# Performance work log

Hardware: AMD Instinct MI355X
Metric: run time of the kernel (lower is better)

Reference implementation:

```python
import jax, jax.numpy as jnp
import numpy as np

B, N, E, DM, DN, H = 8, 128, 2, 128, 128, 4
NEG = -1000000.0


def setup_inputs() -> dict:
    key = jax.random.key(0)
    k1, k2, k3, k4 = jax.random.split(key, 4)
    edge_msgs = jax.random.normal(k1, (B, N, N, E, DM), dtype=jnp.float32)
    node_states = jax.random.normal(k2, (B, N, DN), dtype=jnp.float32)
    edges = jax.random.randint(k3, (B, N, N, E + 1), 0, 2).astype(jnp.int32)
    # Dense(1) kernel per head over concat([edge_msgs, node_states]) -> [H, DM+DN]
    W = jax.random.normal(k4, (H, DM + DN), dtype=jnp.float32) * 0.05
    b = jnp.zeros((H,), dtype=jnp.float32)
    return {"edge_msgs": edge_msgs, "node_states": node_states, "W": W, "b": b, "edges": edges}


def reference(edge_msgs, node_states, W, b, edges):
    Dm = edge_msgs.shape[-1]
    W_msg, W_node = W[:, :Dm], W[:, Dm:]
    # Fused equivalent of tile+concat+Dense(1): split the kernel.
    # s: [B, sender, recv, etype, head]
    s = jnp.einsum('bsrec,hc->bsreh', edge_msgs, W_msg)
    s = s + jnp.einsum('brc,hc->brh', node_states, W_node)[:, None, :, None, :]
    s = jax.nn.elu(s + b)
    # mask: edges[...,1:] is 0/1 over [B,N,N,E]; 0 -> -1e6 bias
    bias = (1.0 - edges[..., 1:].astype(s.dtype)) * NEG  # [B,N,N,E]
    weights = jax.nn.softmax(s + bias[..., None], axis=1)  # softmax over senders
    # weighted sum over senders and edge types, per head: [B, recv, head, Dm]
    out = jnp.einsum('bsreh,bsrec->brhc', weights, edge_msgs)
    Bq, Nq = out.shape[:2]
    return out.reshape(Bq, Nq, -1)  # heads concatenated along last axis
```

## Files before the change

### kernel.cpp

```cpp
#include <hip/hip_runtime.h>
#include <math.h>

#define NB 8
#define NN 128
static constexpr float NEGV = -1000000.0f;

__global__ __launch_bounds__(512, 4)
void edge_attn_kernel(const float* __restrict__ edge_msgs,
                      const float* __restrict__ node_states,
                      const float* __restrict__ W,
                      const float* __restrict__ bvec,
                      const int*   __restrict__ edges,
                      float* __restrict__ out) {
    const int blk = blockIdx.x;
    const int b = blk >> 7;
    const int r = blk & 127;

    const int t  = threadIdx.x;
    const int w  = t >> 6;
    const int l  = t & 63;
    const int e  = l >> 5;
    const int c4 = l & 31;

    __shared__ float part[128 * 68];
    __shared__ float wts [128][2][4];
    __shared__ float ebias[128][2];
    __shared__ float nodep[4];
    __shared__ float outbuf[8][4][128];

    float4 wm0 = *(const float4*)(W +   0 + c4 * 4);
    float4 wm1 = *(const float4*)(W + 256 + c4 * 4);
    float4 wm2 = *(const float4*)(W + 512 + c4 * 4);
    float4 wm3 = *(const float4*)(W + 768 + c4 * 4);

    if (w == 0) {
        float2 nv  = *(const float2*)(node_states + ((size_t)b * NN + r) * 128 + l * 2);
        float2 wn0 = *(const float2*)(W + 128 + l * 2);
        float2 wn1 = *(const float2*)(W + 384 + l * 2);
        float2 wn2 = *(const float2*)(W + 640 + l * 2);
        float2 wn3 = *(const float2*)(W + 896 + l * 2);
        float np0 = nv.x * wn0.x + nv.y * wn0.y;
        float np1 = nv.x * wn1.x + nv.y * wn1.y;
        float np2 = nv.x * wn2.x + nv.y * wn2.y;
        float np3 = nv.x * wn3.x + nv.y * wn3.y;
        #pragma unroll
        for (int m = 32; m >= 1; m >>= 1) {
            np0 += __shfl_xor(np0, m);
            np1 += __shfl_xor(np1, m);
            np2 += __shfl_xor(np2, m);
            np3 += __shfl_xor(np3, m);
        }
        if (l == 0) { nodep[0] = np0; nodep[1] = np1; nodep[2] = np2; nodep[3] = np3; }
    }

    if (t < 256) {
        int s  = t >> 1;
        int ec = t & 1;
        int ev = edges[(((size_t)b * NN + s) * NN + r) * 3 + 1 + ec];
        ebias[s][ec] = (1.0f - (float)ev) * NEGV;
    }

    const float* bp = edge_msgs
        + (size_t)b * (NN * NN * 256)
        + (size_t)r * 256
        + e * 128 + c4 * 4;

    float4 v[16];
    #pragma unroll
    for (int si = 0; si < 16; ++si)
        v[si] = *(const float4*)(bp + (size_t)(w + 8 * si) * 32768);

    const int hsel = l & 3;
    const int g    = (l >> 2) & 7;
    const bool o1  = (l & 1) != 0;
    const bool o2  = (l & 2) != 0;
    #pragma unroll
    for (int si = 0; si < 16; ++si) {
        int s = w + 8 * si;
        float p0 = v[si].x * wm0.x + v[si].y * wm0.y + v[si].z * wm0.z + v[si].w * wm0.w;
        float p1 = v[si].x * wm1.x + v[si].y * wm1.y + v[si].z * wm1.z + v[si].w * wm1.w;
        float p2 = v[si].x * wm2.x + v[si].y * wm2.y + v[si].z * wm2.z + v[si].w * wm2.w;
        float p3 = v[si].x * wm3.x + v[si].y * wm3.y + v[si].z * wm3.z + v[si].w * wm3.w;
        float x01 = o1 ? p1 : p0, y01 = o1 ? p0 : p1;
        float x23 = o1 ? p3 : p2, y23 = o1 ? p2 : p3;
        float r01 = x01 + __shfl_xor(y01, 1);
        float r23 = x23 + __shfl_xor(y23, 1);
        float x2 = o2 ? r23 : r01, y2 = o2 ? r01 : r23;
        float val = x2 + __shfl_xor(y2, 2);
        part[s * 68 + e * 32 + hsel * 8 + g] = val;
    }
    __syncthreads();

    if (t < 256) {
        int p  = t >> 5;
        int j  = t & 31;
        int es = p & 1;
        int h  = p >> 1;
        float bb = bvec[h] + nodep[h];
        float y0, y1, y2, y3;
        #define SCORE(k, dst)                                                  \
        {                                                                      \
            int s = j + 32 * k;                                                \
            const float* q = &part[s * 68 + es * 32 + h * 8];                  \
            float4 qa = *(const float4*)q;                                     \
            float4 qb = *(const float4*)(q + 4);                               \
            float x = (qa.x + qa.y + qa.z + qa.w)                              \
                    + (qb.x + qb.y + qb.z + qb.w) + bb;                        \
            x = x > 0.f ? x : expm1f(x);                                       \
            dst = x + ebias[s][es];                                            \
        }
        SCORE(0, y0) SCORE(1, y1) SCORE(2, y2) SCORE(3, y3)
        #undef SCORE
        float m4 = fmaxf(fmaxf(y0, y1), fmaxf(y2, y3));
        #pragma unroll
        for (int m = 16; m >= 1; m >>= 1) m4 = fmaxf(m4, __shfl_xor(m4, m));
        y0 = __expf(y0 - m4); y1 = __expf(y1 - m4);
        y2 = __expf(y2 - m4); y3 = __expf(y3 - m4);
        float sum = y0 + y1 + y2 + y3;
        #pragma unroll
        for (int m = 16; m >= 1; m >>= 1) sum += __shfl_xor(sum, m);
        float inv = 1.0f / sum;
        wts[j +  0][es][h] = y0 * inv;
        wts[j + 32][es][h] = y1 * inv;
        wts[j + 64][es][h] = y2 * inv;
        wts[j + 96][es][h] = y3 * inv;
    }
    __syncthreads();

    float4 a0 = {0,0,0,0}, a1 = {0,0,0,0}, a2 = {0,0,0,0}, a3 = {0,0,0,0};
    #pragma unroll
    for (int si = 0; si < 16; ++si) {
        int s = w + 8 * si;
        float4 wt = *(const float4*)&wts[s][e][0];
        a0.x += wt.x * v[si].x; a0.y += wt.x * v[si].y; a0.z += wt.x * v[si].z; a0.w += wt.x * v[si].w;
        a1.x += wt.y * v[si].x; a1.y += wt.y * v[si].y; a1.z += wt.y * v[si].z; a1.w += wt.y * v[si].w;
        a2.x += wt.z * v[si].x; a2.y += wt.z * v[si].y; a2.z += wt.z * v[si].z; a2.w += wt.z * v[si].w;
        a3.x += wt.w * v[si].x; a3.y += wt.w * v[si].y; a3.z += wt.w * v[si].z; a3.w += wt.w * v[si].w;
    }
    a0.x += __shfl_xor(a0.x, 32); a0.y += __shfl_xor(a0.y, 32); a0.z += __shfl_xor(a0.z, 32); a0.w += __shfl_xor(a0.w, 32);
    a1.x += __shfl_xor(a1.x, 32); a1.y += __shfl_xor(a1.y, 32); a1.z += __shfl_xor(a1.z, 32); a1.w += __shfl_xor(a1.w, 32);
    a2.x += __shfl_xor(a2.x, 32); a2.y += __shfl_xor(a2.y, 32); a2.z += __shfl_xor(a2.z, 32); a2.w += __shfl_xor(a2.w, 32);
    a3.x += __shfl_xor(a3.x, 32); a3.y += __shfl_xor(a3.y, 32); a3.z += __shfl_xor(a3.z, 32); a3.w += __shfl_xor(a3.w, 32);

    if (e == 0) {
        *(float4*)&outbuf[w][0][c4 * 4] = a0;
        *(float4*)&outbuf[w][1][c4 * 4] = a1;
        *(float4*)&outbuf[w][2][c4 * 4] = a2;
        *(float4*)&outbuf[w][3][c4 * 4] = a3;
    }
    __syncthreads();

    {
        int h = t >> 7;
        int c = t & 127;
        float sv = 0.f;
        #pragma unroll
        for (int k = 0; k < 8; ++k) sv += outbuf[k][h][c];
        out[((size_t)b * NN + r) * 512 + t] = sv;
    }
}

extern "C" void kernel_launch(void* const* d_in, const int* in_sizes, int n_in,
                              void* d_out, int out_size, void* d_ws, size_t ws_size,
                              hipStream_t stream) {
    const float* edge_msgs   = (const float*)d_in[0];
    const float* node_states = (const float*)d_in[1];
    const float* W           = (const float*)d_in[2];
    const float* bvec        = (const float*)d_in[3];
    const int*   edges       = (const int*)d_in[4];
    float* out = (float*)d_out;

    dim3 grid(NB * NN);
    dim3 block(512);
    edge_attn_kernel<<<grid, block, 0, stream>>>(edge_msgs, node_states, W, bvec, edges, out);
}
```

Before: 33.45 us.

## Split work per edge type into separate blocks with a combine kernel

The fused kernel is split by edge type: each 256-thread block handles one (batch, receiver, edge type), writes partial outputs to workspace, and a second kernel sums the two partials. Score reduction now finishes with shuffles instead of a large shared-memory partial buffer, which shrinks shared memory and doubles the block count for better occupancy and latency hiding. The cost is an extra kernel launch plus a write and re-read of a 4 MB partial buffer, and redundant node-state and weight loads per block.

```diff
diff --git a/kernel.cpp b/kernel.cpp
--- a/kernel.cpp
+++ b/kernel.cpp
@@ -5,28 +5,29 @@
 #define NN 128
 static constexpr float NEGV = -1000000.0f;
 
-__global__ __launch_bounds__(512, 4)
-void edge_attn_kernel(const float* __restrict__ edge_msgs,
-                      const float* __restrict__ node_states,
-                      const float* __restrict__ W,
-                      const float* __restrict__ bvec,
-                      const int*   __restrict__ edges,
-                      float* __restrict__ out) {
+__global__ __launch_bounds__(256, 4)
+void edge_attn_partial(const float* __restrict__ edge_msgs,
+                       const float* __restrict__ node_states,
+                       const float* __restrict__ W,
+                       const float* __restrict__ bvec,
+                       const int*   __restrict__ edges,
+                       float* __restrict__ partial) {
     const int blk = blockIdx.x;
-    const int b = blk >> 7;
-    const int r = blk & 127;
+    const int e = blk & 1;
+    const int r = (blk >> 1) & 127;
+    const int b = blk >> 8;
 
-    const int t  = threadIdx.x;
-    const int w  = t >> 6;
-    const int l  = t & 63;
-    const int e  = l >> 5;
-    const int c4 = l & 31;
+    const int t    = threadIdx.x;
+    const int w    = t >> 6;
+    const int l    = t & 63;
+    const int soff = l >> 5;
+    const int c4   = l & 31;
 
-    __shared__ float part[128 * 68];
-    __shared__ float wts [128][2][4];
-    __shared__ float ebias[128][2];
+    __shared__ float sval[128 * 5];
+    __shared__ float wts [128 * 5];
+    __shared__ float ebias[128];
     __shared__ float nodep[4];
-    __shared__ float outbuf[8][4][128];
+    __shared__ float outbuf[4][4][128];
 
     float4 wm0 = *(const float4*)(W +   0 + c4 * 4);
     float4 wm1 = *(const float4*)(W + 256 + c4 * 4);
@@ -53,11 +54,9 @@
         if (l == 0) { nodep[0] = np0; nodep[1] = np1; nodep[2] = np2; nodep[3] = np3; }
     }
 
-    if (t < 256) {
-        int s  = t >> 1;
-        int ec = t & 1;
-        int ev = edges[(((size_t)b * NN + s) * NN + r) * 3 + 1 + ec];
-        ebias[s][ec] = (1.0f - (float)ev) * NEGV;
+    if (t < 128) {
+        int ev = edges[(((size_t)b * NN + t) * NN + r) * 3 + 1 + e];
+        ebias[t] = (1.0f - (float)ev) * NEGV;
     }
 
     const float* bp = edge_msgs
@@ -68,15 +67,14 @@
     float4 v[16];
     #pragma unroll
     for (int si = 0; si < 16; ++si)
-        v[si] = *(const float4*)(bp + (size_t)(w + 8 * si) * 32768);
+        v[si] = *(const float4*)(bp + (size_t)(8 * si + 2 * w + soff) * 32768);
 
     const int hsel = l & 3;
-    const int g    = (l >> 2) & 7;
     const bool o1  = (l & 1) != 0;
     const bool o2  = (l & 2) != 0;
     #pragma unroll
     for (int si = 0; si < 16; ++si) {
-        int s = w + 8 * si;
+        int s = 8 * si + 2 * w + soff;
         float p0 = v[si].x * wm0.x + v[si].y * wm0.y + v[si].z * wm0.z + v[si].w * wm0.w;
         float p1 = v[si].x * wm1.x + v[si].y * wm1.y + v[si].z * wm1.z + v[si].w * wm1.w;
         float p2 = v[si].x * wm2.x + v[si].y * wm2.y + v[si].z * wm2.z + v[si].w * wm2.w;
@@ -87,30 +85,26 @@
         float r23 = x23 + __shfl_xor(y23, 1);
         float x2 = o2 ? r23 : r01, y2 = o2 ? r01 : r23;
         float val = x2 + __shfl_xor(y2, 2);
-        part[s * 68 + e * 32 + hsel * 8 + g] = val;
+        val += __shfl_xor(val, 4);
+        val += __shfl_xor(val, 8);
+        val += __shfl_xor(val, 16);
+        if ((l & 31) < 4)
+            sval[s * 5 + hsel] = val;
     }
     __syncthreads();
 
-    if (t < 256) {
-        int p  = t >> 5;
-        int j  = t & 31;
-        int es = p & 1;
-        int h  = p >> 1;
+    if (t < 128) {
+        int h = t >> 5;
+        int j = t & 31;
         float bb = bvec[h] + nodep[h];
         float y0, y1, y2, y3;
-        #define SCORE(k, dst)                                                  \
-        {                                                                      \
-            int s = j + 32 * k;                                                \
-            const float* q = &part[s * 68 + es * 32 + h * 8];                  \
-            float4 qa = *(const float4*)q;                                     \
-            float4 qb = *(const float4*)(q + 4);                               \
-            float x = (qa.x + qa.y + qa.z + qa.w)                              \
-                    + (qb.x + qb.y + qb.z + qb.w) + bb;                        \
-            x = x > 0.f ? x : expm1f(x);                                       \
-            dst = x + ebias[s][es];                                            \
+        {
+            float x;
+            x = sval[(j +  0) * 5 + h] + bb; x = x > 0.f ? x : expm1f(x); y0 = x + ebias[j +  0];
+            x = sval[(j + 32) * 5 + h] + bb; x = x > 0.f ? x : expm1f(x); y1 = x + ebias[j + 32];
+            x = sval[(j + 64) * 5 + h] + bb; x = x > 0.f ? x : expm1f(x); y2 = x + ebias[j + 64];
+            x = sval[(j + 96) * 5 + h] + bb; x = x > 0.f ? x : expm1f(x); y3 = x + ebias[j + 96];
         }
-        SCORE(0, y0) SCORE(1, y1) SCORE(2, y2) SCORE(3, y3)
-        #undef SCORE
         float m4 = fmaxf(fmaxf(y0, y1), fmaxf(y2, y3));
         #pragma unroll
         for (int m = 16; m >= 1; m >>= 1) m4 = fmaxf(m4, __shfl_xor(m4, m));
@@ -120,29 +114,32 @@
         #pragma unroll
         for (int m = 16; m >= 1; m >>= 1) sum += __shfl_xor(sum, m);
         float inv = 1.0f / sum;
-        wts[j +  0][es][h] = y0 * inv;
-        wts[j + 32][es][h] = y1 * inv;
-        wts[j + 64][es][h] = y2 * inv;
-        wts[j + 96][es][h] = y3 * inv;
+        wts[(j +  0) * 5 + h] = y0 * inv;
+        wts[(j + 32) * 5 + h] = y1 * inv;
+        wts[(j + 64) * 5 + h] = y2 * inv;
+        wts[(j + 96) * 5 + h] = y3 * inv;
     }
     __syncthreads();
 
     float4 a0 = {0,0,0,0}, a1 = {0,0,0,0}, a2 = {0,0,0,0}, a3 = {0,0,0,0};
     #pragma unroll
     for (int si = 0; si < 16; ++si) {
-        int s = w + 8 * si;
-        float4 wt = *(const float4*)&wts[s][e][0];
-        a0.x += wt.x * v[si].x; a0.y += wt.x * v[si].y; a0.z += wt.x * v[si].z; a0.w += wt.x * v[si].w;
-        a1.x += wt.y * v[si].x; a1.y += wt.y * v[si].y; a1.z += wt.y * v[si].z; a1.w += wt.y * v[si].w;
-        a2.x += wt.z * v[si].x; a2.y += wt.z * v[si].y; a2.z += wt.z * v[si].z; a2.w += wt.z * v[si].w;
-        a3.x += wt.w * v[si].x; a3.y += wt.w * v[si].y; a3.z += wt.w * v[si].z; a3.w += wt.w * v[si].w;
+        int s = 8 * si + 2 * w + soff;
+        float w0 = wts[s * 5 + 0];
+        float w1 = wts[s * 5 + 1];
+        float w2 = wts[s * 5 + 2];
+        float w3 = wts[s * 5 + 3];
+        a0.x += w0 * v[si].x; a0.y += w0 * v[si].y; a0.z += w0 * v[si].z; a0.w += w0 * v[si].w;
+        a1.x += w1 * v[si].x; a1.y += w1 * v[si].y; a1.z += w1 * v[si].z; a1.w += w1 * v[si].w;
+        a2.x += w2 * v[si].x; a2.y += w2 * v[si].y; a2.z += w2 * v[si].z; a2.w += w2 * v[si].w;
+        a3.x += w3 * v[si].x; a3.y += w3 * v[si].y; a3.z += w3 * v[si].z; a3.w += w3 * v[si].w;
     }
     a0.x += __shfl_xor(a0.x, 32); a0.y += __shfl_xor(a0.y, 32); a0.z += __shfl_xor(a0.z, 32); a0.w += __shfl_xor(a0.w, 32);
     a1.x += __shfl_xor(a1.x, 32); a1.y += __shfl_xor(a1.y, 32); a1.z += __shfl_xor(a1.z, 32); a1.w += __shfl_xor(a1.w, 32);
     a2.x += __shfl_xor(a2.x, 32); a2.y += __shfl_xor(a2.y, 32); a2.z += __shfl_xor(a2.z, 32); a2.w += __shfl_xor(a2.w, 32);
     a3.x += __shfl_xor(a3.x, 32); a3.y += __shfl_xor(a3.y, 32); a3.z += __shfl_xor(a3.z, 32); a3.w += __shfl_xor(a3.w, 32);
 
-    if (e == 0) {
+    if (soff == 0) {
         *(float4*)&outbuf[w][0][c4 * 4] = a0;
         *(float4*)&outbuf[w][1][c4 * 4] = a1;
         *(float4*)&outbuf[w][2][c4 * 4] = a2;
@@ -150,14 +147,23 @@
     }
     __syncthreads();
 
-    {
-        int h = t >> 7;
-        int c = t & 127;
-        float sv = 0.f;
-        #pragma unroll
-        for (int k = 0; k < 8; ++k) sv += outbuf[k][h][c];
-        out[((size_t)b * NN + r) * 512 + t] = sv;
+    #pragma unroll
+    for (int k = 0; k < 2; ++k) {
+        int idx = t + 256 * k;
+        int h = idx >> 7;
+        int c = idx & 127;
+        float sv = outbuf[0][h][c] + outbuf[1][h][c] + outbuf[2][h][c] + outbuf[3][h][c];
+        partial[((size_t)e * NB * NN + (size_t)b * NN + r) * 512 + idx] = sv;
     }
+}
+
+__global__ __launch_bounds__(256)
+void edge_attn_combine(const float* __restrict__ partial, float* __restrict__ out) {
+    int i = blockIdx.x * 256 + threadIdx.x;
+    float4 p0 = *(const float4*)(partial + (size_t)i * 4);
+    float4 p1 = *(const float4*)(partial + 524288 + (size_t)i * 4);
+    float4 o; o.x = p0.x + p1.x; o.y = p0.y + p1.y; o.z = p0.z + p1.z; o.w = p0.w + p1.w;
+    *(float4*)(out + (size_t)i * 4) = o;
 }
 
 extern "C" void kernel_launch(void* const* d_in, const int* in_sizes, int n_in,
@@ -168,9 +174,10 @@
     const float* W           = (const float*)d_in[2];
     const float* bvec        = (const float*)d_in[3];
     const int*   edges       = (const int*)d_in[4];
-    float* out = (float*)d_out;
+    float* out     = (float*)d_out;
+    float* partial = (float*)d_ws;
 
-    dim3 grid(NB * NN);
-    dim3 block(512);
-    edge_attn_kernel<<<grid, block, 0, stream>>>(edge_msgs, node_states, W, bvec, edges, out);
+    edge_attn_partial<<<dim3(NB * NN * 2), dim3(256), 0, stream>>>(
+        edge_msgs, node_states, W, bvec, edges, partial);
+    edge_attn_combine<<<dim3(131072 / 256), dim3(256), 0, stream>>>(partial, out);
 }
```

Measured after the change: 40.03 us. +19.7%, slower.

## Stream senders in tiles with online softmax and double-buffered register loads

Applied to the files above, without the earlier changes.

Each block now runs 256 threads instead of 512. It walks the 128 senders in four tiles of 32, prefetching the next tile into a second register buffer while it computes the current one. Softmax becomes an online (running max and sum) update, rescaling the accumulators with per-head correction factors, so the full score buffer and the 16-deep register array are no longer needed. The intent is to cut register and LDS pressure and overlap memory loads with compute, at the cost of a few more syncthreads per tile and extra shuffle reductions.

```diff
diff --git a/kernel.cpp b/kernel.cpp
--- a/kernel.cpp
+++ b/kernel.cpp
@@ -5,7 +5,7 @@
 #define NN 128
 static constexpr float NEGV = -1000000.0f;
 
-__global__ __launch_bounds__(512, 4)
+__global__ __launch_bounds__(256, 4)
 void edge_attn_kernel(const float* __restrict__ edge_msgs,
                       const float* __restrict__ node_states,
                       const float* __restrict__ W,
@@ -22,16 +22,33 @@
     const int e  = l >> 5;
     const int c4 = l & 31;
 
-    __shared__ float part[128 * 68];
-    __shared__ float wts [128][2][4];
-    __shared__ float ebias[128][2];
+    const int g  = t >> 5;
+    const int j  = t & 31;
+    const int se = g & 1;
+    const int sh = g >> 1;
+
+    __shared__ float sval[32 * 9];
+    __shared__ float wtile[32 * 9];
+    __shared__ float ebias[128 * 2];
     __shared__ float nodep[4];
-    __shared__ float outbuf[8][4][128];
+    __shared__ float corrbuf[8];
+    __shared__ float lbuf[8];
+    __shared__ float outbuf[4][4][128];
 
     float4 wm0 = *(const float4*)(W +   0 + c4 * 4);
     float4 wm1 = *(const float4*)(W + 256 + c4 * 4);
     float4 wm2 = *(const float4*)(W + 512 + c4 * 4);
     float4 wm3 = *(const float4*)(W + 768 + c4 * 4);
+
+    const float* bp = edge_msgs
+        + (size_t)b * (NN * NN * 256)
+        + (size_t)r * 256
+        + e * 128 + c4 * 4;
+
+    float4 v[2][8];
+    #pragma unroll
+    for (int si = 0; si < 8; ++si)
+        v[0][si] = *(const float4*)(bp + (size_t)(8 * w + si) * 32768);
 
     if (w == 0) {
         float2 nv  = *(const float2*)(node_states + ((size_t)b * NN + r) * 128 + l * 2);
@@ -53,89 +70,110 @@
         if (l == 0) { nodep[0] = np0; nodep[1] = np1; nodep[2] = np2; nodep[3] = np3; }
     }
 
-    if (t < 256) {
+    {
         int s  = t >> 1;
         int ec = t & 1;
         int ev = edges[(((size_t)b * NN + s) * NN + r) * 3 + 1 + ec];
-        ebias[s][ec] = (1.0f - (float)ev) * NEGV;
-    }
-
-    const float* bp = edge_msgs
-        + (size_t)b * (NN * NN * 256)
-        + (size_t)r * 256
-        + e * 128 + c4 * 4;
-
-    float4 v[16];
+        ebias[s * 2 + ec] = (1.0f - (float)ev) * NEGV;
+    }
+    __syncthreads();
+
+    const float bb = bvec[sh] + nodep[sh];
+
+    float m_run = -INFINITY, l_run = 0.0f;
+    float4 a0 = {0,0,0,0}, a1 = {0,0,0,0}, a2 = {0,0,0,0}, a3 = {0,0,0,0};
+
+    const int  hsel = l & 3;
+    const bool o1   = (l & 1) != 0;
+    const bool o2   = (l & 2) != 0;
+
     #pragma unroll
-    for (int si = 0; si < 16; ++si)
-        v[si] = *(const float4*)(bp + (size_t)(w + 8 * si) * 32768);
-
-    const int hsel = l & 3;
-    const int g    = (l >> 2) & 7;
-    const bool o1  = (l & 1) != 0;
-    const bool o2  = (l & 2) != 0;
-    #pragma unroll
-    for (int si = 0; si < 16; ++si) {
-        int s = w + 8 * si;
-        float p0 = v[si].x * wm0.x + v[si].y * wm0.y + v[si].z * wm0.z + v[si].w * wm0.w;
-        float p1 = v[si].x * wm1.x + v[si].y * wm1.y + v[si].z * wm1.z + v[si].w * wm1.w;
-        float p2 = v[si].x * wm2.x + v[si].y * wm2.y + v[si].z * wm2.z + v[si].w * wm2.w;
-        float p3 = v[si].x * wm3.x + v[si].y * wm3.y + v[si].z * wm3.z + v[si].w * wm3.w;
-        float x01 = o1 ? p1 : p0, y01 = o1 ? p0 : p1;
-        float x23 = o1 ? p3 : p2, y23 = o1 ? p2 : p3;
-        float r01 = x01 + __shfl_xor(y01, 1);
-        float r23 = x23 + __shfl_xor(y23, 1);
-        float x2 = o2 ? r23 : r01, y2 = o2 ? r01 : r23;
-        float val = x2 + __shfl_xor(y2, 2);
-        part[s * 68 + e * 32 + hsel * 8 + g] = val;
-    }
+    for (int T = 0; T < 4; ++T) {
+        const int cur = T & 1;
+        const int nxt = cur ^ 1;
+        if (T < 3) {
+            #pragma unroll
+            for (int si = 0; si < 8; ++si)
+                v[nxt][si] = *(const float4*)(bp + (size_t)(32 * (T + 1) + 8 * w + si) * 32768);
+        }
+        #pragma unroll
+        for (int si = 0; si < 8; ++si) {
+            float4 d = v[cur][si];
+            float p0 = d.x * wm0.x + d.y * wm0.y + d.z * wm0.z + d.w * wm0.w;
+            float p1 = d.x * wm1.x + d.y * wm1.y + d.z * wm1.z + d.w * wm1.w;
+            float p2 = d.x * wm2.x + d.y * wm2.y + d.z * wm2.z + d.w * wm2.w;
+            float p3 = d.x * wm3.x + d.y * wm3.y + d.z * wm3.z + d.w * wm3.w;
+            float x01 = o1 ? p1 : p0, y01 = o1 ? p0 : p1;
+            float x23 = o1 ? p3 : p2, y23 = o1 ? p2 : p3;
+            float r01 = x01 + __shfl_xor(y01, 1);
+            float r23 = x23 + __shfl_xor(y23, 1);
+            float x2 = o2 ? r23 : r01, y2 = o2 ? r01 : r23;
+            float val = x2 + __shfl_xor(y2, 2);
+            val += __shfl_xor(val, 4);
+            val += __shfl_xor(val, 8);
+            val += __shfl_xor(val, 16);
+            if ((l & 31) < 4)
+                sval[(8 * w + si) * 9 + e * 4 + hsel] = val;
+        }
+        __syncthreads();
+
+        {
+            float x = sval[j * 9 + se * 4 + sh] + bb;
+            x = x > 0.f ? x : expm1f(x);
+            float y = x + ebias[(32 * T + j) * 2 + se];
+            float mt = y;
+            #pragma unroll
+            for (int m = 16; m >= 1; m >>= 1) mt = fmaxf(mt, __shfl_xor(mt, m));
+            float m_new = fmaxf(m_run, mt);
+            float corr  = __expf(m_run - m_new);
+            float p     = __expf(y - m_new);
+            float ls = p;
+            #pragma unroll
+            for (int m = 16; m >= 1; m >>= 1) ls += __shfl_xor(ls, m);
+            l_run = l_run * corr + ls;
+            m_run = m_new;
+            wtile[j * 9 + se * 4 + sh] = p;
+            if (j == 0) corrbuf[sh * 2 + se] = corr;
+        }
+        __syncthreads();
+
+        {
+            float c0 = corrbuf[0 * 2 + e];
+            float c1 = corrbuf[1 * 2 + e];
+            float c2 = corrbuf[2 * 2 + e];
+            float c3 = corrbuf[3 * 2 + e];
+            a0.x *= c0; a0.y *= c0; a0.z *= c0; a0.w *= c0;
+            a1.x *= c1; a1.y *= c1; a1.z *= c1; a1.w *= c1;
+            a2.x *= c2; a2.y *= c2; a2.z *= c2; a2.w *= c2;
+            a3.x *= c3; a3.y *= c3; a3.z *= c3; a3.w *= c3;
+            #pragma unroll
+            for (int si = 0; si < 8; ++si) {
+                int sl = 8 * w + si;
+                float4 d = v[cur][si];
+                float w0 = wtile[sl * 9 + e * 4 + 0];
+                float w1 = wtile[sl * 9 + e * 4 + 1];
+                float w2 = wtile[sl * 9 + e * 4 + 2];
+                float w3 = wtile[sl * 9 + e * 4 + 3];
+                a0.x += w0 * d.x; a0.y += w0 * d.y; a0.z += w0 * d.z; a0.w += w0 * d.w;
+                a1.x += w1 * d.x; a1.y += w1 * d.y; a1.z += w1 * d.z; a1.w += w1 * d.w;
+                a2.x += w2 * d.x; a2.y += w2 * d.y; a2.z += w2 * d.z; a2.w += w2 * d.w;
+                a3.x += w3 * d.x; a3.y += w3 * d.y; a3.z += w3 * d.z; a3.w += w3 * d.w;
+            }
+        }
+        __syncthreads();
+    }
+
+    if (j == 0) lbuf[sh * 2 + se] = l_run;
     __syncthreads();
-
-    if (t < 256) {
-        int p  = t >> 5;
-        int j  = t & 31;
-        int es = p & 1;
-        int h  = p >> 1;
-        float bb = bvec[h] + nodep[h];
-        float y0, y1, y2, y3;
-        #define SCORE(k, dst)                                                  \
-        {                                                                      \
-            int s = j + 32 * k;                                                \
-            const float* q = &part[s * 68 + es * 32 + h * 8];                  \
-            float4 qa = *(const float4*)q;                                     \
-            float4 qb = *(const float4*)(q + 4);                               \
-            float x = (qa.x + qa.y + qa.z + qa.w)                              \
-                    + (qb.x + qb.y + qb.z + qb.w) + bb;                        \
-            x = x > 0.f ? x : expm1f(x);                                       \
-            dst = x + ebias[s][es];                                            \
-        }
-        SCORE(0, y0) SCORE(1, y1) SCORE(2, y2) SCORE(3, y3)
-        #undef SCORE
-        float m4 = fmaxf(fmaxf(y0, y1), fmaxf(y2, y3));
-        #pragma unroll
-        for (int m = 16; m >= 1; m >>= 1) m4 = fmaxf(m4, __shfl_xor(m4, m));
-        y0 = __expf(y0 - m4); y1 = __expf(y1 - m4);
-        y2 = __expf(y2 - m4); y3 = __expf(y3 - m4);
-        float sum = y0 + y1 + y2 + y3;
-        #pragma unroll
-        for (int m = 16; m >= 1; m >>= 1) sum += __shfl_xor(sum, m);
-        float inv = 1.0f / sum;
-        wts[j +  0][es][h] = y0 * inv;
-        wts[j + 32][es][h] = y1 * inv;
-        wts[j + 64][es][h] = y2 * inv;
-        wts[j + 96][es][h] = y3 * inv;
-    }
-    __syncthreads();
-
-    float4 a0 = {0,0,0,0}, a1 = {0,0,0,0}, a2 = {0,0,0,0}, a3 = {0,0,0,0};
-    #pragma unroll
-    for (int si = 0; si < 16; ++si) {
-        int s = w + 8 * si;
-        float4 wt = *(const float4*)&wts[s][e][0];
-        a0.x += wt.x * v[si].x; a0.y += wt.x * v[si].y; a0.z += wt.x * v[si].z; a0.w += wt.x * v[si].w;
-        a1.x += wt.y * v[si].x; a1.y += wt.y * v[si].y; a1.z += wt.y * v[si].z; a1.w += wt.y * v[si].w;
-        a2.x += wt.z * v[si].x; a2.y += wt.z * v[si].y; a2.z += wt.z * v[si].z; a2.w += wt.z * v[si].w;
-        a3.x += wt.w * v[si].x; a3.y += wt.w * v[si].y; a3.z += wt.w * v[si].z; a3.w += wt.w * v[si].w;
+    {
+        float i0 = 1.0f / lbuf[0 * 2 + e];
+        float i1 = 1.0f / lbuf[1 * 2 + e];
+        float i2 = 1.0f / lbuf[2 * 2 + e];
+        float i3 = 1.0f / lbuf[3 * 2 + e];
+        a0.x *= i0; a0.y *= i0; a0.z *= i0; a0.w *= i0;
+        a1.x *= i1; a1.y *= i1; a1.z *= i1; a1.w *= i1;
+        a2.x *= i2; a2.y *= i2; a2.z *= i2; a2.w *= i2;
+        a3.x *= i3; a3.y *= i3; a3.z *= i3; a3.w *= i3;
     }
     a0.x += __shfl_xor(a0.x, 32); a0.y += __shfl_xor(a0.y, 32); a0.z += __shfl_xor(a0.z, 32); a0.w += __shfl_xor(a0.w, 32);
     a1.x += __shfl_xor(a1.x, 32); a1.y += __shfl_xor(a1.y, 32); a1.z += __shfl_xor(a1.z, 32); a1.w += __shfl_xor(a1.w, 32);
@@ -150,13 +188,13 @@
     }
     __syncthreads();
 
-    {
-        int h = t >> 7;
-        int c = t & 127;
-        float sv = 0.f;
-        #pragma unroll
-        for (int k = 0; k < 8; ++k) sv += outbuf[k][h][c];
-        out[((size_t)b * NN + r) * 512 + t] = sv;
+    #pragma unroll
+    for (int k = 0; k < 2; ++k) {
+        int idx = t + 256 * k;
+        int h = idx >> 7;
+        int c = idx & 127;
+        float sv = outbuf[0][h][c] + outbuf[1][h][c] + outbuf[2][h][c] + outbuf[3][h][c];
+        out[((size_t)b * NN + r) * 512 + idx] = sv;
     }
 }
 
@@ -170,7 +208,6 @@
     const int*   edges       = (const int*)d_in[4];
     float* out = (float*)d_out;
 
-    dim3 grid(NB * NN);
-    dim3 block(512);
-    edge_attn_kernel<<<grid, block, 0, stream>>>(edge_msgs, node_states, W, bvec, edges, out);
+    edge_attn_kernel<<<dim3(NB * NN), dim3(256), 0, stream>>>(
+        edge_msgs, node_states, W, bvec, edges, out);
 }
```

Result: slower. 120.2 us (+259.3%).
